# Optimization experiments

Hardware: AMD Instinct MI355X
Metric: run time of the kernel (lower is better)

Reference implementation:

```python
import jax, jax.numpy as jnp
import numpy as np

EPS_BN = 1e-5


def setup_inputs() -> dict:
    key = jax.random.key(0)
    ks = jax.random.split(key, 6)
    n, L, D, G = 10000, 256, 32, 3
    return {
        "pop": jax.random.normal(ks[0], (n, L), dtype=jnp.float32),
        "conv_w": jax.random.normal(ks[1], (D, 1, 1), dtype=jnp.float32) * 0.1,
        "conv_b": jnp.zeros((D,), dtype=jnp.float32),
        "bn_gamma": jnp.ones((D,), dtype=jnp.float32),
        "bn_beta": jnp.zeros((D,), dtype=jnp.float32),
        "gcn_ws": jax.random.normal(ks[2], (G, D, D), dtype=jnp.float32) * (1.0 / np.sqrt(D)),
        "gcn_bs": jnp.zeros((G, D), dtype=jnp.float32),
        "out_w": jax.random.normal(ks[3], (D, 3), dtype=jnp.float32) * (1.0 / np.sqrt(D)),
        "out_b": jnp.zeros((3,), dtype=jnp.float32),
        "k": 32,
    }


def _knn_edges(x, k):
    # x: [n, d]. PyG knn_graph(loop=False): edges (neighbor j -> center i).
    n = x.shape[0]
    sq = jnp.sum(x * x, axis=-1)  # [n]
    d2 = sq[:, None] + sq[None, :] - 2.0 * (x @ x.T)  # [n, n]
    idx = jnp.arange(n)
    d2 = d2.at[idx, idx].set(jnp.inf)  # exclude self (loop=False)
    _, nbr = jax.lax.top_k(-d2, k)  # [n, k] nearest neighbors of each node
    src = nbr.reshape(-1)                       # sources (neighbors)
    dst = jnp.repeat(idx, k)                    # targets (centers)
    return src, dst


def _gcn(x, W, b, src, dst, deg_isqrt):
    # GCNConv with self-loops already folded into (src, dst) and deg.
    h = x @ W  # [n, D_out]
    norm = deg_isqrt[src] * deg_isqrt[dst]  # [E]
    msg = h[src] * norm[:, None]
    agg = jax.ops.segment_sum(msg, dst, num_segments=x.shape[0])
    return agg + b


def reference(pop, conv_w, conv_b, bn_gamma, bn_beta, gcn_ws, gcn_bs, out_w, out_b, k):
    n, L = pop.shape
    # --- stem: Conv1d(1, D, kernel=1) -> y[n, c, l] = pop[n, l] * w[c] + b[c]
    w = conv_w[:, 0, 0]  # [D]
    y = pop[:, None, :] * w[None, :, None] + conv_b[None, :, None]  # [n, D, L]
    # --- BatchNorm1d (training mode: batch stats over (N, L), biased var)
    mean = jnp.mean(y, axis=(0, 2))
    var = jnp.mean(jnp.square(y - mean[None, :, None]), axis=(0, 2))
    y = (y - mean[None, :, None]) * (bn_gamma / jnp.sqrt(var + EPS_BN))[None, :, None] + bn_beta[None, :, None]
    y = jax.nn.silu(y)
    # --- adaptive avg pool to length 1 -> mean over L
    x = jnp.mean(y, axis=-1)  # [n, D]
    # --- knn graph on pooled features
    src, dst = _knn_edges(x, k)
    # add self loops (GCNConv default)
    idx = jnp.arange(n)
    src_f = jnp.concatenate([src, idx])
    dst_f = jnp.concatenate([dst, idx])
    deg = jax.ops.segment_sum(jnp.ones_like(dst_f, dtype=x.dtype), dst_f, num_segments=n)
    deg_isqrt = jnp.where(deg > 0, 1.0 / jnp.sqrt(deg), 0.0)
    # --- stacked GCNs
    for i in range(gcn_ws.shape[0]):
        x = _gcn(x, gcn_ws[i], gcn_bs[i], src_f, dst_f, deg_isqrt)
        x = jax.nn.silu(x)
    x = _gcn(x, out_w, out_b, src_f, dst_f, deg_isqrt)  # [n, 3]
    return jax.nn.softmax(x, axis=-1)
```

## Files before the change

kernel.cpp:

```cpp
#include <hip/hip_runtime.h>
#include <math.h>

#define N_NODES 10000
#define NPAD    10016
#define L_LEN   256
#define D_DIM   32
#define K_NBR   32
#define NTOT    (N_NODES * L_LEN)
#define EPS_BN  1e-5f
#define QB      3
#define BT      1024
#define SD      3

typedef unsigned int uint4_ev __attribute__((ext_vector_type(4)));

__device__ __forceinline__ float silu_f(float x) {
    return x / (1.0f + expf(-x));
}

__global__ void stats_kernel(const float* __restrict__ pop, float* __restrict__ stats) {
    __shared__ float s1[256], s2[256];
    int t = threadIdx.x;
    float a = 0.f, b = 0.f;
    for (int idx = blockIdx.x * 256 + t; idx < NTOT; idx += gridDim.x * 256) {
        float v = pop[idx];
        a += v; b += v * v;
    }
    s1[t] = a; s2[t] = b;
    __syncthreads();
    for (int s = 128; s > 0; s >>= 1) {
        if (t < s) { s1[t] += s1[t + s]; s2[t] += s2[t + s]; }
        __syncthreads();
    }
    if (t == 0) { atomicAdd(&stats[0], s1[0]); atomicAdd(&stats[1], s2[0]); }
}

__global__ void feat_kernel(const float* __restrict__ pop,
                            const float* __restrict__ conv_w,
                            const float* __restrict__ conv_b,
                            const float* __restrict__ gamma,
                            const float* __restrict__ beta,
                            const float* __restrict__ stats,
                            float* __restrict__ X,
                            float* __restrict__ XT,
                            float* __restrict__ SQ) {
    __shared__ float row[L_LEN];
    __shared__ float part[256];
    int i = blockIdx.x;
    int t = threadIdx.x;
    row[t] = pop[i * L_LEN + t];
    __syncthreads();
    int d = t & 31, g = t >> 5;
    float M  = stats[0] * (1.0f / NTOT);
    float Vc = stats[1] * (1.0f / NTOT) - M * M;
    float w = conv_w[d], b = conv_b[d];
    float mean = fmaf(w, M, b);
    float var  = w * w * Vc;
    float sc = gamma[d] / sqrtf(var + EPS_BN);
    float bt = beta[d];
    float acc = 0.f;
    int l0 = g * 32;
    #pragma unroll
    for (int l = 0; l < 32; ++l) {
        float y = fmaf(row[l0 + l], w, b);
        float z = fmaf(y - mean, sc, bt);
        acc += silu_f(z);
    }
    part[t] = acc;
    __syncthreads();
    if (t < 32) {
        float s = 0.f;
        #pragma unroll
        for (int gg = 0; gg < 8; ++gg) s += part[gg * 32 + t];
        float xv = s * (1.0f / L_LEN);
        X[i * D_DIM + t] = xv;
        XT[t * N_NODES + i] = xv;
        part[t] = xv;
    }
    __syncthreads();
    if (t == 0) {
        float sq = 0.f;
        #pragma unroll
        for (int dd = 0; dd < 32; ++dd) sq += part[dd] * part[dd];
        SQ[i] = sq;
    }
}

__global__ __launch_bounds__(BT) void knn3_kernel(const float* __restrict__ X,
                                                  const float* __restrict__ XT,
                                                  const float* __restrict__ SQ,
                                                  int* __restrict__ NBR) {
    extern __shared__ unsigned int keys[];
    __shared__ float qv[QB][D_DIM];
    __shared__ float sqq[QB];
    __shared__ unsigned int whist[16][256];
    __shared__ unsigned int wmin[16], wmax[16];
    __shared__ unsigned int gkmin[QB], gkmax[QB], gkth[QB];
    __shared__ int gwant[QB], gcnt[QB];

    int t = threadIdx.x;
    int lane = t & 63;
    int w = t >> 6;
    int q0 = blockIdx.x * QB;

    if (t < QB * D_DIM) {
        int q = t >> 5, d = t & 31;
        int gq_ = q0 + q;
        qv[q][d] = (gq_ < N_NODES) ? X[gq_ * D_DIM + d] : 0.f;
    }
    if (t < QB) sqq[t] = (q0 + t < N_NODES) ? SQ[q0 + t] : 0.f;
    __syncthreads();

    float acc[QB][SD * 4];
    #pragma unroll
    for (int q = 0; q < QB; ++q)
        #pragma unroll
        for (int s = 0; s < SD * 4; ++s) acc[q][s] = 0.f;

    #pragma unroll 2
    for (int d = 0; d < D_DIM; ++d) {
        float qd0 = qv[0][d], qd1 = qv[1][d], qd2 = qv[2][d];
        const float4* xr4 = (const float4*)(XT + d * N_NODES);
        #pragma unroll
        for (int s = 0; s < SD; ++s) {
            int i4 = t + s * BT;
            float4 xv = make_float4(0.f, 0.f, 0.f, 0.f);
            if (i4 < N_NODES / 4) xv = xr4[i4];
            acc[0][s * 4 + 0] = fmaf(qd0, xv.x, acc[0][s * 4 + 0]);
            acc[0][s * 4 + 1] = fmaf(qd0, xv.y, acc[0][s * 4 + 1]);
            acc[0][s * 4 + 2] = fmaf(qd0, xv.z, acc[0][s * 4 + 2]);
            acc[0][s * 4 + 3] = fmaf(qd0, xv.w, acc[0][s * 4 + 3]);
            acc[1][s * 4 + 0] = fmaf(qd1, xv.x, acc[1][s * 4 + 0]);
            acc[1][s * 4 + 1] = fmaf(qd1, xv.y, acc[1][s * 4 + 1]);
            acc[1][s * 4 + 2] = fmaf(qd1, xv.z, acc[1][s * 4 + 2]);
            acc[1][s * 4 + 3] = fmaf(qd1, xv.w, acc[1][s * 4 + 3]);
            acc[2][s * 4 + 0] = fmaf(qd2, xv.x, acc[2][s * 4 + 0]);
            acc[2][s * 4 + 1] = fmaf(qd2, xv.y, acc[2][s * 4 + 1]);
            acc[2][s * 4 + 2] = fmaf(qd2, xv.z, acc[2][s * 4 + 2]);
            acc[2][s * 4 + 3] = fmaf(qd2, xv.w, acc[2][s * 4 + 3]);
        }
    }

    const float4* sq4p = (const float4*)SQ;
    #pragma unroll
    for (int s = 0; s < SD; ++s) {
        int i4 = t + s * BT;
        int j4 = 4 * i4;
        if (j4 < NPAD) {
            float4 sj = make_float4(0.f, 0.f, 0.f, 0.f);
            if (i4 < N_NODES / 4) sj = sq4p[i4];
            float sjv[4] = { sj.x, sj.y, sj.z, sj.w };
            #pragma unroll
            for (int q = 0; q < QB; ++q) {
                int gq_ = q0 + q;
                unsigned int kk[4];
                #pragma unroll
                for (int jj = 0; jj < 4; ++jj) {
                    int j = j4 + jj;
                    unsigned int kv = 0xFFFFFFFFu;
                    if (j < N_NODES && gq_ < N_NODES && j != gq_) {
                        float d2 = (sqq[q] + sjv[jj]) - 2.0f * acc[q][s * 4 + jj];
                        unsigned int u = __float_as_uint(d2);
                        u ^= (u & 0x80000000u) ? 0xFFFFFFFFu : 0x80000000u;
                        kv = u;
                    }
                    kk[jj] = kv;
                }
                uint4_ev wv = { kk[0], kk[1], kk[2], kk[3] };
                *(uint4_ev*)&keys[q * NPAD + j4] = wv;
            }
        }
    }
    __syncthreads();

    int g     = (w >= 10) ? 2 : (w >= 5 ? 1 : 0);
    int wbase = (g == 2) ? 10 : g * 5;
    int gsz   = (g == 2) ? 6 : 5;
    int lt    = (w - wbase) * 64 + lane;
    int GT    = gsz * 64;
    unsigned int* kq = keys + g * NPAD;
    int gq = q0 + g;

    unsigned int mn = 0xFFFFFFFFu, mx = 0u;
    for (int j = lt; j < NPAD; j += GT) {
        unsigned int u = kq[j];
        mn = mn < u ? mn : u;
        if (u != 0xFFFFFFFFu) mx = mx > u ? mx : u;
    }
    #pragma unroll
    for (int off = 32; off > 0; off >>= 1) {
        unsigned int a = (unsigned int)__shfl_xor((int)mn, off);
        unsigned int b = (unsigned int)__shfl_xor((int)mx, off);
        mn = mn < a ? mn : a;
        mx = mx > b ? mx : b;
    }
    if (lane == 0) { wmin[w] = mn; wmax[w] = mx; }
    __syncthreads();
    if (t < QB) {
        int b0 = (t == 2) ? 10 : t * 5;
        int bs = (t == 2) ? 6 : 5;
        unsigned int m0 = 0xFFFFFFFFu, m1 = 0u;
        for (int k = 0; k < bs; ++k) {
            m0 = m0 < wmin[b0 + k] ? m0 : wmin[b0 + k];
            m1 = m1 > wmax[b0 + k] ? m1 : wmax[b0 + k];
        }
        gkmin[t] = m0; gkmax[t] = m1;
        gkth[t] = m0; gwant[t] = K_NBR; gcnt[t] = 0;
    }
    __syncthreads();

    for (int shift = 24; shift >= 0; shift -= 8) {
        unsigned int gdiff = gkmin[g] ^ gkmax[g];
        bool skip = (gdiff >> shift) == 0;
        if (!skip) {
            #pragma unroll
            for (int b = lane; b < 256; b += 64) whist[w][b] = 0u;
            unsigned int kth = gkth[g];
            int sh8 = shift + 8;
            for (int j = lt; j < NPAD; j += GT) {
                unsigned int u = kq[j];
                if (((unsigned long long)u >> sh8) == ((unsigned long long)kth >> sh8))
                    atomicAdd(&whist[w][(u >> shift) & 255u], 1u);
            }
        }
        __syncthreads();
        if (!skip && w == wbase) {
            int want = gwant[g];
            unsigned int kth = gkth[g];
            unsigned int c[4]; unsigned int gsum = 0u;
            #pragma unroll
            for (int i = 0; i < 4; ++i) {
                unsigned int tot = 0u; int b = 4 * lane + i;
                for (int k = 0; k < gsz; ++k) tot += whist[wbase + k][b];
                c[i] = tot; gsum += tot;
            }
            unsigned int x = gsum;
            #pragma unroll
            for (int off = 1; off < 64; off <<= 1) {
                unsigned int y = (unsigned int)__shfl_up((int)x, off);
                if (lane >= off) x += y;
            }
            unsigned int e = x - gsum;
            #pragma unroll
            for (int i = 0; i < 4; ++i) {
                if (e < (unsigned int)want && (unsigned int)want <= e + c[i]) {
                    gwant[g] = want - (int)e;
                    gkth[g] = (kth & ~(255u << shift)) |
                              ((unsigned int)(4 * lane + i) << shift);
                }
                e += c[i];
            }
        }
        __syncthreads();
    }

    unsigned int kth = gkth[g];
    int wantEq = gwant[g];
    int baseSlot = K_NBR - wantEq;
    if (gq < N_NODES) {
        for (int j = lt; j < NPAD; j += GT) {
            if (kq[j] < kth) {
                int p = atomicAdd(&gcnt[g], 1);
                NBR[gq * K_NBR + p] = j;
            }
        }
        if (w == wbase) {
            int last = -1;
            for (int e = 0; e < wantEq; ++e) {
                unsigned int best = 0xFFFFFFFFu;
                for (int j = lane; j < NPAD; j += 64) {
                    if (kq[j] == kth && j > last && (unsigned int)j < best)
                        best = (unsigned int)j;
                }
                #pragma unroll
                for (int off = 32; off > 0; off >>= 1) {
                    unsigned int o = (unsigned int)__shfl_xor((int)best, off);
                    best = best < o ? best : o;
                }
                if (lane == 0) NBR[gq * K_NBR + baseSlot + e] = (int)best;
                last = (int)best;
            }
        }
    }
}

__global__ void gcn_fused(const float* __restrict__ Xin, const int* __restrict__ NBR,
                          const float* __restrict__ W, const float* __restrict__ bias,
                          float* __restrict__ Xout) {
    __shared__ float Ws[D_DIM * D_DIM];
    __shared__ float sAgg[8][D_DIM];
    __shared__ int nb[8][K_NBR];
    int t = threadIdx.x, g = t >> 5, d = t & 31;
    #pragma unroll
    for (int q = 0; q < 4; ++q) Ws[q * 256 + t] = W[q * 256 + t];
    int i = blockIdx.x * 8 + g;
    nb[g][d] = NBR[i * K_NBR + d];
    __syncthreads();
    float s = Xin[i * D_DIM + d];
    #pragma unroll 8
    for (int e = 0; e < K_NBR; ++e) s += Xin[nb[g][e] * D_DIM + d];
    sAgg[g][d] = s;
    __syncthreads();
    float acc = 0.f;
    #pragma unroll
    for (int m = 0; m < D_DIM; ++m)
        acc = fmaf(sAgg[g][m], Ws[m * D_DIM + d], acc);
    float v = fmaf(acc, 1.0f / 33.0f, bias[d]);
    Xout[i * D_DIM + d] = silu_f(v);
}

__global__ void out_final(const float* __restrict__ Xin, const int* __restrict__ NBR,
                          const float* __restrict__ Wout, const float* __restrict__ out_b,
                          float* __restrict__ out) {
    __shared__ float Ws[D_DIM * 3];
    __shared__ float sAgg[8][D_DIM];
    __shared__ int nb[8][K_NBR];
    int t = threadIdx.x, g = t >> 5, d = t & 31;
    if (t < D_DIM * 3) Ws[t] = Wout[t];
    int i = blockIdx.x * 8 + g;
    nb[g][d] = NBR[i * K_NBR + d];
    __syncthreads();
    float s = Xin[i * D_DIM + d];
    #pragma unroll 8
    for (int e = 0; e < K_NBR; ++e) s += Xin[nb[g][e] * D_DIM + d];
    sAgg[g][d] = s;
    __syncthreads();
    if (d < 3) {
        float v[3];
        #pragma unroll
        for (int c = 0; c < 3; ++c) {
            float a = 0.f;
            #pragma unroll
            for (int m = 0; m < D_DIM; ++m) a = fmaf(sAgg[g][m], Ws[m * 3 + c], a);
            v[c] = fmaf(a, 1.0f / 33.0f, out_b[c]);
        }
        float mx = fmaxf(v[0], fmaxf(v[1], v[2]));
        float e0 = expf(v[0] - mx), e1 = expf(v[1] - mx), e2 = expf(v[2] - mx);
        out[i * 3 + d] = expf(v[d] - mx) / (e0 + e1 + e2);
    }
}

extern "C" void kernel_launch(void* const* d_in, const int* in_sizes, int n_in,
                              void* d_out, int out_size, void* d_ws, size_t ws_size,
                              hipStream_t stream) {
    const float* pop    = (const float*)d_in[0];
    const float* conv_w = (const float*)d_in[1];
    const float* conv_b = (const float*)d_in[2];
    const float* gamma  = (const float*)d_in[3];
    const float* beta   = (const float*)d_in[4];
    const float* gcn_ws = (const float*)d_in[5];
    const float* gcn_bs = (const float*)d_in[6];
    const float* out_w  = (const float*)d_in[7];
    const float* out_b  = (const float*)d_in[8];

    char* ws = (char*)d_ws;
    const size_t o_stats = 0;
    const size_t o_X     = 256;
    const size_t o_XT    = o_X + 1280000;
    const size_t o_SQ    = o_XT + 1280000;
    const size_t o_H     = o_SQ + 40192;
    const size_t o_NBR   = o_H + 1280000;

    float* stats = (float*)(ws + o_stats);
    float* X     = (float*)(ws + o_X);
    float* XT    = (float*)(ws + o_XT);
    float* SQ    = (float*)(ws + o_SQ);
    float* H     = (float*)(ws + o_H);
    int*   NBR   = (int*)  (ws + o_NBR);
    float* out   = (float*)d_out;

    (void)hipMemsetAsync(stats, 0, 2 * sizeof(float), stream);
    stats_kernel<<<512, 256, 0, stream>>>(pop, stats);
    feat_kernel<<<N_NODES, 256, 0, stream>>>(pop, conv_w, conv_b, gamma, beta, stats, X, XT, SQ);

    const int nqb = (N_NODES + QB - 1) / QB;
    const size_t keys_bytes = (size_t)QB * NPAD * 4;
    knn3_kernel<<<nqb, BT, keys_bytes, stream>>>(X, XT, SQ, NBR);

    gcn_fused<<<N_NODES / 8, 256, 0, stream>>>(X, NBR, gcn_ws,        gcn_bs,      H);
    gcn_fused<<<N_NODES / 8, 256, 0, stream>>>(H, NBR, gcn_ws + 1024, gcn_bs + 32, X);
    gcn_fused<<<N_NODES / 8, 256, 0, stream>>>(X, NBR, gcn_ws + 2048, gcn_bs + 64, H);
    out_final<<<N_NODES / 8, 256, 0, stream>>>(H, NBR, out_w, out_b, out);
}
```

Baseline: 948.9 us.

## Replace radix-select kNN with per-wave streaming top-k insertion

The block-per-3-queries kNN kernel, which wrote all distances into shared memory and ran a multi-pass radix histogram select, is replaced by a kernel where each wavefront handles 4 queries. The wave streams candidates 64 at a time and keeps a sorted running top-64 list in registers, inserting keys with ballot and shuffle. This removes the large shared-memory buffer, the block-wide barriers and the transposed XT copy. The cost is that every query block now reads all of X with row-strided, uncoalesced loads. Insertion also becomes serial per candidate, which is cheap only if few candidates beat the current maximum.

```diff
diff --git a/kernel.cpp b/kernel.cpp
--- a/kernel.cpp
+++ b/kernel.cpp
@@ -2,17 +2,11 @@
 #include <math.h>
 
 #define N_NODES 10000
-#define NPAD    10016
 #define L_LEN   256
 #define D_DIM   32
 #define K_NBR   32
 #define NTOT    (N_NODES * L_LEN)
 #define EPS_BN  1e-5f
-#define QB      3
-#define BT      1024
-#define SD      3
-
-typedef unsigned int uint4_ev __attribute__((ext_vector_type(4)));
 
 __device__ __forceinline__ float silu_f(float x) {
     return x / (1.0f + expf(-x));
@@ -42,7 +36,6 @@
                             const float* __restrict__ beta,
                             const float* __restrict__ stats,
                             float* __restrict__ X,
-                            float* __restrict__ XT,
                             float* __restrict__ SQ) {
     __shared__ float row[L_LEN];
     __shared__ float part[256];
@@ -74,7 +67,6 @@
         for (int gg = 0; gg < 8; ++gg) s += part[gg * 32 + t];
         float xv = s * (1.0f / L_LEN);
         X[i * D_DIM + t] = xv;
-        XT[t * N_NODES + i] = xv;
         part[t] = xv;
     }
     __syncthreads();
@@ -86,201 +78,92 @@
     }
 }
 
-__global__ __launch_bounds__(BT) void knn3_kernel(const float* __restrict__ X,
-                                                  const float* __restrict__ XT,
-                                                  const float* __restrict__ SQ,
-                                                  int* __restrict__ NBR) {
-    extern __shared__ unsigned int keys[];
-    __shared__ float qv[QB][D_DIM];
-    __shared__ float sqq[QB];
-    __shared__ unsigned int whist[16][256];
-    __shared__ unsigned int wmin[16], wmax[16];
-    __shared__ unsigned int gkmin[QB], gkmax[QB], gkth[QB];
-    __shared__ int gwant[QB], gcnt[QB];
-
-    int t = threadIdx.x;
-    int lane = t & 63;
-    int w = t >> 6;
-    int q0 = blockIdx.x * QB;
-
-    if (t < QB * D_DIM) {
-        int q = t >> 5, d = t & 31;
-        int gq_ = q0 + q;
-        qv[q][d] = (gq_ < N_NODES) ? X[gq_ * D_DIM + d] : 0.f;
-    }
-    if (t < QB) sqq[t] = (q0 + t < N_NODES) ? SQ[q0 + t] : 0.f;
-    __syncthreads();
-
-    float acc[QB][SD * 4];
-    #pragma unroll
-    for (int q = 0; q < QB; ++q)
-        #pragma unroll
-        for (int s = 0; s < SD * 4; ++s) acc[q][s] = 0.f;
-
-    #pragma unroll 2
-    for (int d = 0; d < D_DIM; ++d) {
-        float qd0 = qv[0][d], qd1 = qv[1][d], qd2 = qv[2][d];
-        const float4* xr4 = (const float4*)(XT + d * N_NODES);
-        #pragma unroll
-        for (int s = 0; s < SD; ++s) {
-            int i4 = t + s * BT;
-            float4 xv = make_float4(0.f, 0.f, 0.f, 0.f);
-            if (i4 < N_NODES / 4) xv = xr4[i4];
-            acc[0][s * 4 + 0] = fmaf(qd0, xv.x, acc[0][s * 4 + 0]);
-            acc[0][s * 4 + 1] = fmaf(qd0, xv.y, acc[0][s * 4 + 1]);
-            acc[0][s * 4 + 2] = fmaf(qd0, xv.z, acc[0][s * 4 + 2]);
-            acc[0][s * 4 + 3] = fmaf(qd0, xv.w, acc[0][s * 4 + 3]);
-            acc[1][s * 4 + 0] = fmaf(qd1, xv.x, acc[1][s * 4 + 0]);
-            acc[1][s * 4 + 1] = fmaf(qd1, xv.y, acc[1][s * 4 + 1]);
-            acc[1][s * 4 + 2] = fmaf(qd1, xv.z, acc[1][s * 4 + 2]);
-            acc[1][s * 4 + 3] = fmaf(qd1, xv.w, acc[1][s * 4 + 3]);
-            acc[2][s * 4 + 0] = fmaf(qd2, xv.x, acc[2][s * 4 + 0]);
-            acc[2][s * 4 + 1] = fmaf(qd2, xv.y, acc[2][s * 4 + 1]);
-            acc[2][s * 4 + 2] = fmaf(qd2, xv.z, acc[2][s * 4 + 2]);
-            acc[2][s * 4 + 3] = fmaf(qd2, xv.w, acc[2][s * 4 + 3]);
-        }
-    }
-
-    const float4* sq4p = (const float4*)SQ;
-    #pragma unroll
-    for (int s = 0; s < SD; ++s) {
-        int i4 = t + s * BT;
-        int j4 = 4 * i4;
-        if (j4 < NPAD) {
-            float4 sj = make_float4(0.f, 0.f, 0.f, 0.f);
-            if (i4 < N_NODES / 4) sj = sq4p[i4];
-            float sjv[4] = { sj.x, sj.y, sj.z, sj.w };
+__device__ __forceinline__ void insert_top(unsigned long long &run,
+                                           unsigned long long key, int lane) {
+    unsigned long long kmax = __shfl(run, 63);
+    unsigned long long mask = __ballot(key < kmax);
+    while (mask) {
+        int b = (int)__ffsll(mask) - 1;
+        mask &= mask - 1;
+        unsigned long long kb = __shfl(key, b);
+        if (kb < kmax) {
+            int pos = __popcll(__ballot(run <= kb));
+            unsigned long long up = __shfl_up(run, 1);
+            run = (lane < pos) ? run : (lane == pos ? kb : up);
+            kmax = __shfl(run, 63);
+        }
+    }
+}
+
+__global__ __launch_bounds__(256) void knn_wave(const float* __restrict__ X,
+                                                const float* __restrict__ SQ,
+                                                int* __restrict__ NBR) {
+    int lane = threadIdx.x & 63;
+    int wv   = threadIdx.x >> 6;
+    int q0   = blockIdx.x * 16 + wv * 4;
+
+    const float4* qr0 = (const float4*)(X + (size_t)(q0 + 0) * D_DIM);
+    const float4* qr1 = (const float4*)(X + (size_t)(q0 + 1) * D_DIM);
+    const float4* qr2 = (const float4*)(X + (size_t)(q0 + 2) * D_DIM);
+    const float4* qr3 = (const float4*)(X + (size_t)(q0 + 3) * D_DIM);
+    float sq0 = SQ[q0 + 0], sq1 = SQ[q0 + 1], sq2 = SQ[q0 + 2], sq3 = SQ[q0 + 3];
+
+    unsigned long long run0 = ~0ULL, run1 = ~0ULL, run2 = ~0ULL, run3 = ~0ULL;
+
+    for (int base = 0; base < N_NODES; base += 64) {
+        int c = base + lane;
+        bool valid = c < N_NODES;
+        float4 xr[8];
+        const float4* xp = (const float4*)(X + (size_t)c * D_DIM);
+        if (valid) {
             #pragma unroll
-            for (int q = 0; q < QB; ++q) {
-                int gq_ = q0 + q;
-                unsigned int kk[4];
-                #pragma unroll
-                for (int jj = 0; jj < 4; ++jj) {
-                    int j = j4 + jj;
-                    unsigned int kv = 0xFFFFFFFFu;
-                    if (j < N_NODES && gq_ < N_NODES && j != gq_) {
-                        float d2 = (sqq[q] + sjv[jj]) - 2.0f * acc[q][s * 4 + jj];
-                        unsigned int u = __float_as_uint(d2);
-                        u ^= (u & 0x80000000u) ? 0xFFFFFFFFu : 0x80000000u;
-                        kv = u;
-                    }
-                    kk[jj] = kv;
-                }
-                uint4_ev wv = { kk[0], kk[1], kk[2], kk[3] };
-                *(uint4_ev*)&keys[q * NPAD + j4] = wv;
-            }
-        }
-    }
-    __syncthreads();
-
-    int g     = (w >= 10) ? 2 : (w >= 5 ? 1 : 0);
-    int wbase = (g == 2) ? 10 : g * 5;
-    int gsz   = (g == 2) ? 6 : 5;
-    int lt    = (w - wbase) * 64 + lane;
-    int GT    = gsz * 64;
-    unsigned int* kq = keys + g * NPAD;
-    int gq = q0 + g;
-
-    unsigned int mn = 0xFFFFFFFFu, mx = 0u;
-    for (int j = lt; j < NPAD; j += GT) {
-        unsigned int u = kq[j];
-        mn = mn < u ? mn : u;
-        if (u != 0xFFFFFFFFu) mx = mx > u ? mx : u;
-    }
-    #pragma unroll
-    for (int off = 32; off > 0; off >>= 1) {
-        unsigned int a = (unsigned int)__shfl_xor((int)mn, off);
-        unsigned int b = (unsigned int)__shfl_xor((int)mx, off);
-        mn = mn < a ? mn : a;
-        mx = mx > b ? mx : b;
-    }
-    if (lane == 0) { wmin[w] = mn; wmax[w] = mx; }
-    __syncthreads();
-    if (t < QB) {
-        int b0 = (t == 2) ? 10 : t * 5;
-        int bs = (t == 2) ? 6 : 5;
-        unsigned int m0 = 0xFFFFFFFFu, m1 = 0u;
-        for (int k = 0; k < bs; ++k) {
-            m0 = m0 < wmin[b0 + k] ? m0 : wmin[b0 + k];
-            m1 = m1 > wmax[b0 + k] ? m1 : wmax[b0 + k];
-        }
-        gkmin[t] = m0; gkmax[t] = m1;
-        gkth[t] = m0; gwant[t] = K_NBR; gcnt[t] = 0;
-    }
-    __syncthreads();
-
-    for (int shift = 24; shift >= 0; shift -= 8) {
-        unsigned int gdiff = gkmin[g] ^ gkmax[g];
-        bool skip = (gdiff >> shift) == 0;
-        if (!skip) {
+            for (int i = 0; i < 8; ++i) xr[i] = xp[i];
+        } else {
             #pragma unroll
-            for (int b = lane; b < 256; b += 64) whist[w][b] = 0u;
-            unsigned int kth = gkth[g];
-            int sh8 = shift + 8;
-            for (int j = lt; j < NPAD; j += GT) {
-                unsigned int u = kq[j];
-                if (((unsigned long long)u >> sh8) == ((unsigned long long)kth >> sh8))
-                    atomicAdd(&whist[w][(u >> shift) & 255u], 1u);
-            }
-        }
-        __syncthreads();
-        if (!skip && w == wbase) {
-            int want = gwant[g];
-            unsigned int kth = gkth[g];
-            unsigned int c[4]; unsigned int gsum = 0u;
-            #pragma unroll
-            for (int i = 0; i < 4; ++i) {
-                unsigned int tot = 0u; int b = 4 * lane + i;
-                for (int k = 0; k < gsz; ++k) tot += whist[wbase + k][b];
-                c[i] = tot; gsum += tot;
-            }
-            unsigned int x = gsum;
-            #pragma unroll
-            for (int off = 1; off < 64; off <<= 1) {
-                unsigned int y = (unsigned int)__shfl_up((int)x, off);
-                if (lane >= off) x += y;
-            }
-            unsigned int e = x - gsum;
-            #pragma unroll
-            for (int i = 0; i < 4; ++i) {
-                if (e < (unsigned int)want && (unsigned int)want <= e + c[i]) {
-                    gwant[g] = want - (int)e;
-                    gkth[g] = (kth & ~(255u << shift)) |
-                              ((unsigned int)(4 * lane + i) << shift);
-                }
-                e += c[i];
-            }
-        }
-        __syncthreads();
-    }
-
-    unsigned int kth = gkth[g];
-    int wantEq = gwant[g];
-    int baseSlot = K_NBR - wantEq;
-    if (gq < N_NODES) {
-        for (int j = lt; j < NPAD; j += GT) {
-            if (kq[j] < kth) {
-                int p = atomicAdd(&gcnt[g], 1);
-                NBR[gq * K_NBR + p] = j;
-            }
-        }
-        if (w == wbase) {
-            int last = -1;
-            for (int e = 0; e < wantEq; ++e) {
-                unsigned int best = 0xFFFFFFFFu;
-                for (int j = lane; j < NPAD; j += 64) {
-                    if (kq[j] == kth && j > last && (unsigned int)j < best)
-                        best = (unsigned int)j;
-                }
-                #pragma unroll
-                for (int off = 32; off > 0; off >>= 1) {
-                    unsigned int o = (unsigned int)__shfl_xor((int)best, off);
-                    best = best < o ? best : o;
-                }
-                if (lane == 0) NBR[gq * K_NBR + baseSlot + e] = (int)best;
-                last = (int)best;
-            }
-        }
+            for (int i = 0; i < 8; ++i) xr[i] = make_float4(0.f, 0.f, 0.f, 0.f);
+        }
+        float sqc = valid ? SQ[c] : 0.f;
+
+        float a0 = 0.f, a1 = 0.f, a2 = 0.f, a3 = 0.f;
+        #pragma unroll
+        for (int i = 0; i < 8; ++i) {
+            float4 v  = xr[i];
+            float4 w0 = qr0[i];
+            float4 w1 = qr1[i];
+            float4 w2 = qr2[i];
+            float4 w3 = qr3[i];
+            a0 = fmaf(v.x, w0.x, a0); a0 = fmaf(v.y, w0.y, a0);
+            a0 = fmaf(v.z, w0.z, a0); a0 = fmaf(v.w, w0.w, a0);
+            a1 = fmaf(v.x, w1.x, a1); a1 = fmaf(v.y, w1.y, a1);
+            a1 = fmaf(v.z, w1.z, a1); a1 = fmaf(v.w, w1.w, a1);
+            a2 = fmaf(v.x, w2.x, a2); a2 = fmaf(v.y, w2.y, a2);
+            a2 = fmaf(v.z, w2.z, a2); a2 = fmaf(v.w, w2.w, a2);
+            a3 = fmaf(v.x, w3.x, a3); a3 = fmaf(v.y, w3.y, a3);
+            a3 = fmaf(v.z, w3.z, a3); a3 = fmaf(v.w, w3.w, a3);
+        }
+
+        #pragma unroll
+        for (int qi = 0; qi < 4; ++qi) {
+            float sqq = (qi == 0) ? sq0 : (qi == 1) ? sq1 : (qi == 2) ? sq2 : sq3;
+            float acc = (qi == 0) ? a0  : (qi == 1) ? a1  : (qi == 2) ? a2  : a3;
+            float d2 = (sqq + sqc) - 2.0f * acc;
+            unsigned int u = __float_as_uint(d2);
+            u ^= (u & 0x80000000u) ? 0xFFFFFFFFu : 0x80000000u;
+            unsigned long long key =
+                ((unsigned long long)u << 32) | (unsigned int)c;
+            if (!valid || c == q0 + qi) key = ~0ULL;
+            if      (qi == 0) insert_top(run0, key, lane);
+            else if (qi == 1) insert_top(run1, key, lane);
+            else if (qi == 2) insert_top(run2, key, lane);
+            else              insert_top(run3, key, lane);
+        }
+    }
+
+    if (lane < K_NBR) {
+        NBR[(size_t)(q0 + 0) * K_NBR + lane] = (int)(run0 & 0xFFFFFFFFULL);
+        NBR[(size_t)(q0 + 1) * K_NBR + lane] = (int)(run1 & 0xFFFFFFFFULL);
+        NBR[(size_t)(q0 + 2) * K_NBR + lane] = (int)(run2 & 0xFFFFFFFFULL);
+        NBR[(size_t)(q0 + 3) * K_NBR + lane] = (int)(run3 & 0xFFFFFFFFULL);
     }
 }
 
@@ -356,14 +239,12 @@
     char* ws = (char*)d_ws;
     const size_t o_stats = 0;
     const size_t o_X     = 256;
-    const size_t o_XT    = o_X + 1280000;
-    const size_t o_SQ    = o_XT + 1280000;
+    const size_t o_SQ    = o_X + 1280000;
     const size_t o_H     = o_SQ + 40192;
     const size_t o_NBR   = o_H + 1280000;
 
     float* stats = (float*)(ws + o_stats);
     float* X     = (float*)(ws + o_X);
-    float* XT    = (float*)(ws + o_XT);
     float* SQ    = (float*)(ws + o_SQ);
     float* H     = (float*)(ws + o_H);
     int*   NBR   = (int*)  (ws + o_NBR);
@@ -371,11 +252,9 @@
 
     (void)hipMemsetAsync(stats, 0, 2 * sizeof(float), stream);
     stats_kernel<<<512, 256, 0, stream>>>(pop, stats);
-    feat_kernel<<<N_NODES, 256, 0, stream>>>(pop, conv_w, conv_b, gamma, beta, stats, X, XT, SQ);
-
-    const int nqb = (N_NODES + QB - 1) / QB;
-    const size_t keys_bytes = (size_t)QB * NPAD * 4;
-    knn3_kernel<<<nqb, BT, keys_bytes, stream>>>(X, XT, SQ, NBR);
+    feat_kernel<<<N_NODES, 256, 0, stream>>>(pop, conv_w, conv_b, gamma, beta, stats, X, SQ);
+
+    knn_wave<<<N_NODES / 16, 256, 0, stream>>>(X, SQ, NBR);
 
     gcn_fused<<<N_NODES / 8, 256, 0, stream>>>(X, NBR, gcn_ws,        gcn_bs,      H);
     gcn_fused<<<N_NODES / 8, 256, 0, stream>>>(H, NBR, gcn_ws + 1024, gcn_bs + 32, X);
```

Measured after the change: 1.071 ms. 1.13x slower.
